# Performance work log

Hardware: AMD Instinct MI355X
Metric: run time of the kernel (lower is better)

## Reference

```python
import jax, jax.numpy as jnp
import numpy as np

# ExLoss constants (use_prior=False path)
T = 10.0
W_BU, W_H, W_TH = 1.0, 1.0, 3.0
P_MARGIN, N_MARGIN = 0.2, 0.3

B, C, D = 32, 40000, 2048


def setup_inputs() -> dict:
    key = jax.random.key(0)
    k1, k2, k3, k4 = jax.random.split(key, 4)
    inputs = jax.random.normal(k1, (B, D), dtype=jnp.float32)
    targets = jax.random.randint(k2, (B,), 0, 16)            # few identities -> positive pairs exist
    indexs = jax.random.randint(k3, (B,), 0, C)              # unused (use_prior=False)
    label_to_pairs = jnp.zeros((B,), dtype=jnp.int32)        # unused placeholder
    V = jax.random.normal(k4, (C, D), dtype=jnp.float32)
    V = V / jnp.linalg.norm(V, axis=1, keepdims=True)        # bank rows are L2-normalized by the EMA update
    return {"inputs": inputs, "V": V, "targets": targets,
            "label_to_pairs": label_to_pairs, "indexs": indexs}


def _masked_bce(logits, mask, target):
    # BCEWithLogits, reduction='mean' over masked elements; 0 if mask empty
    # per-elem: target*softplus(-x) + (1-target)*softplus(x)
    per = target * jax.nn.softplus(-logits) + (1.0 - target) * jax.nn.softplus(logits)
    cnt = jnp.sum(mask)
    s = jnp.sum(jnp.where(mask, per, 0.0))
    return jnp.where(cnt > 0, s / jnp.maximum(cnt, 1), 0.0)


def _ex_loss(inputs, V, targets):
    n = inputs.shape[0]
    # Exclusive: memory-bank matmul, scaled by t
    outputs = (inputs @ V.T) * T                                   # [B, C]
    # bu_loss: cross entropy (mean)
    logp = jax.nn.log_softmax(outputs, axis=1)
    bu_loss = -jnp.mean(jnp.take_along_axis(logp, targets[:, None], axis=1))

    # hard_negative_mining (batch sims, off-diagonal)
    ni = inputs / jnp.linalg.norm(inputs, axis=1, keepdims=True)
    sims = ni @ ni.T                                               # [B, B]
    eye = jnp.eye(n, dtype=bool)
    same = targets[:, None] == targets[None, :]
    pos = same & ~eye                                              # positive pairs, diag removed
    neg = ~same                                                    # negatives (diag is always 'same')
    # n_thrds: row min of psims BEFORE 2->-2 replacement (fill=2 where not positive)
    n_thrds = jnp.min(jnp.where(pos, sims, 2.0), axis=1, keepdims=True) - N_MARGIN
    # p_thrds: row max after 2->-2 replacement (fill=-2 where not positive)
    p_thrds = jnp.max(jnp.where(pos, sims, -2.0), axis=1, keepdims=True) - P_MARGIN
    hp_mask = pos & (sims < p_thrds)        # fill value 2 can never be < p_thrds (<= 0.8)
    hn_mask = neg & (sims > n_thrds)        # fill value -2 can never be > n_thrds
    h_loss = _masked_bce(sims, hp_mask, 1.0) + _masked_bce(sims, hn_mask, 0.0)

    # hard_negative_mining_with_table (only if no zero rows in V)
    active = jnp.all(jnp.sum(V, axis=1) != 0)
    nV = ni @ V.T                                                  # [B, C]
    n_th_t = jnp.take_along_axis(nV, targets[:, None], axis=1) - N_MARGIN  # [B,1]
    nsims_t = V[targets] @ V.T                                     # [B, C]
    t_mask = (n_th_t < nsims_t) & (nsims_t < 0.9999)
    th_loss = jnp.where(active, _masked_bce(nsims_t, t_mask, 0.0), 0.0)

    loss = W_BU * bu_loss + W_H * h_loss + W_TH * th_loss
    return loss, outputs


def reference(inputs, V, targets, label_to_pairs, indexs):
    # label_to_pairs / indexs unused: use_prior=False in ExLoss.__init__
    return _ex_loss(inputs, V, targets)
```

## Files before the change

### kernel.cpp

```cpp
#include <hip/hip_runtime.h>
#include <math.h>

#define B_ 32
#define C_ 40000
#define D_ 2048
#define T_SCALE 10.0f
#define P_MARG 0.2f
#define N_MARG 0.3f
#define NSTEP 64
#define KSPL 4
#define NCB 625
#define NBLK (NCB * KSPL)

typedef __attribute__((ext_vector_type(4))) float f32x4;
typedef __fp16 fp16x2 __attribute__((ext_vector_type(2)));
typedef _Float16 f16x2n __attribute__((ext_vector_type(2)));
typedef _Float16 half8_t __attribute__((ext_vector_type(8)));

#define OP1_OFF 0
#define OP_FLOATS (B_ * C_)
#define NS0_OFF (OP1_OFF + 3 * OP_FLOATS)
#define VR_OFF (NS0_OFF + 4 * OP_FLOATS)
#define VR_FLOATS C_
#define SC_OFF (VR_OFF + VR_FLOATS)
#define S_HLOSS 0
#define S_THSUM 1
#define S_THCNT 2
#define S_BAD 3
#define S_NTH 4
#define S_BU 36
#define SC_FLOATS 128
#define DT_OFF (SC_OFF + SC_FLOATS)
#define DT_FLOATS (32 * 32)
#define AF_OFF (DT_OFF + DT_FLOATS)
#define AF_FLOATS (NSTEP * 2048 / 2)
#define WS_FLOATS_TOTAL (AF_OFF + AF_FLOATS)

__device__ __forceinline__ float softplus_f(float x) {
    return (x > 0.f) ? (x + log1pf(expf(-x))) : log1pf(expf(x));
}

__device__ __forceinline__ void split_f16x2(float x0, float x1, unsigned& uh, unsigned& ul) {
    fp16x2 h = __builtin_amdgcn_cvt_pkrtz(x0, x1);
    float r0 = x0 - (float)h[0];
    float r1 = x1 - (float)h[1];
    fp16x2 lo = __builtin_amdgcn_cvt_pkrtz(r0, r1);
    uh = __builtin_bit_cast(unsigned, h);
    ul = __builtin_bit_cast(unsigned, lo);
}

__device__ __forceinline__ unsigned pack_rtne(float x0, float x1) {
    f16x2n p = {(_Float16)x0, (_Float16)x1};
    return __builtin_bit_cast(unsigned, p);
}

__global__ __launch_bounds__(256) void build_Afrag(const float* __restrict__ in,
                                                   const float* __restrict__ V,
                                                   const int* __restrict__ tgt,
                                                   unsigned short* __restrict__ Af) {
    int s = blockIdx.x;
    int f = threadIdx.x >> 6;
    int l = threadIdx.x & 63;
    int row = f * 16 + (l & 15);
    int k = s * 32 + (l >> 4) * 8;
    const float* src = (row < 32) ? (in + (size_t)row * D_ + k)
                                  : (V + (size_t)tgt[row - 32] * D_ + k);
    f32x4 x0 = *(const f32x4*)src;
    f32x4 x1 = *(const f32x4*)(src + 4);
    uint4 u = make_uint4(pack_rtne(x0[0], x0[1]), pack_rtne(x0[2], x0[3]),
                         pack_rtne(x1[0], x1[1]), pack_rtne(x1[2], x1[3]));
    *(uint4*)(Af + (size_t)s * 2048 + (size_t)f * 512 + (size_t)l * 8) = u;
}

__global__ __launch_bounds__(256) void sims_dots(const float* __restrict__ in,
                                                 float* __restrict__ dt) {
    __shared__ float part[8][32];
    int i = blockIdx.x;
    int j = threadIdx.x & 31;
    int sl = threadIdx.x >> 5;
    const float4* a4 = (const float4*)(in + (size_t)i * D_ + sl * 256);
    const float4* b4 = (const float4*)(in + (size_t)j * D_ + sl * 256);
    float s = 0.f;
#pragma unroll 4
    for (int k = 0; k < 64; ++k) {
        float4 x = a4[k], y = b4[k];
        s += x.x * y.x + x.y * y.y + x.z * y.z + x.w * y.w;
    }
    part[sl][j] = s;
    __syncthreads();
    if (threadIdx.x < 32) {
        float t = 0.f;
#pragma unroll
        for (int p = 0; p < 8; ++p) t += part[p][threadIdx.x];
        dt[i * 32 + threadIdx.x] = t;
    }
}

__global__ __launch_bounds__(1024) void small_finish(const float* __restrict__ in,
                                                     const float* __restrict__ V,
                                                     const int* __restrict__ tgt,
                                                     float* __restrict__ ws) {
    __shared__ float sims[32][33];
    __shared__ float nthr[32], pthr[32];
    __shared__ int ts[32];
    __shared__ float diag[32];
    __shared__ float red[4];
    int tid = threadIdx.x;
    int i = tid >> 5, j = tid & 31;
    const float* dt = ws + DT_OFF;
    if (tid < 32) { ts[tid] = tgt[tid]; diag[tid] = dt[tid * 32 + tid]; }
    if (tid < 4) red[tid] = 0.f;
    __syncthreads();
    float sim = dt[i * 32 + j] * rsqrtf(diag[i] * diag[j]);
    sims[i][j] = sim;
    __syncthreads();
    if (tid < 32) {
        float nmin = 2.f, pmax = -2.f;
        int ti = ts[tid];
        for (int jj = 0; jj < 32; ++jj) {
            bool pos = (ts[jj] == ti) && (jj != tid);
            float v = sims[tid][jj];
            if (pos) { nmin = fminf(nmin, v); pmax = fmaxf(pmax, v); }
        }
        nthr[tid] = nmin - N_MARG;
        pthr[tid] = pmax - P_MARG;
    }
    __syncthreads();
    bool pos = (ts[i] == ts[j]) && (i != j);
    bool neg = (ts[i] != ts[j]);
    if (pos && sim < pthr[i]) { atomicAdd(&red[0], softplus_f(-sim)); atomicAdd(&red[1], 1.f); }
    if (neg && sim > nthr[i]) { atomicAdd(&red[2], softplus_f(sim)); atomicAdd(&red[3], 1.f); }

    const float4* a4 = (const float4*)(in + (size_t)i * D_);
    const float4* v4 = (const float4*)(V + (size_t)ts[i] * D_);
    float sn = 0.f;
    for (int k = j; k < D_ / 4; k += 32) {
        float4 x = a4[k], y = v4[k];
        sn += x.x * y.x + x.y * y.y + x.z * y.z + x.w * y.w;
    }
    for (int off = 16; off > 0; off >>= 1) sn += __shfl_down(sn, off, 32);
    if (j == 0) ws[SC_OFF + S_NTH + i] = sn * rsqrtf(diag[i]) - N_MARG;
    __syncthreads();
    if (tid == 0) {
        float h = 0.f;
        if (red[1] > 0.f) h += red[0] / red[1];
        if (red[3] > 0.f) h += red[2] / red[3];
        ws[SC_OFF + S_HLOSS] = h;
    }
}

__global__ __launch_bounds__(256, 6) void gemm_mfma(const float* __restrict__ V,
                                                    const unsigned short* __restrict__ Af,
                                                    float* __restrict__ op0,
                                                    float* __restrict__ ws) {
    const int l = threadIdx.x & 63;
    const int w = threadIdx.x >> 6;
    const int ks = blockIdx.x / NCB;
    const int cb = blockIdx.x % NCB;
    const int col = l & 15, g = l >> 4;
    const int c = (cb * 4 + w) * 16 + col;

    const float* vp = V + (size_t)c * D_ + ks * 512 + g * 8;
    const unsigned short* ap = Af + (size_t)(ks * 16) * 2048 + (size_t)l * 8;

    f32x4 z = {0.f, 0.f, 0.f, 0.f};
    f32x4 acc0 = z, acc1 = z, acc2 = z, acc3 = z;
    float vsum = 0.f;

#pragma unroll
    for (int s = 0; s < 16; ++s) {
        const unsigned short* as = ap + (size_t)s * 2048;
        uint4 a0 = *(const uint4*)(as + 0 * 512);
        uint4 a1 = *(const uint4*)(as + 1 * 512);
        uint4 a2 = *(const uint4*)(as + 2 * 512);
        uint4 a3 = *(const uint4*)(as + 3 * 512);
        f32x4 v0 = *(const f32x4*)(vp + s * 32);
        f32x4 v1 = *(const f32x4*)(vp + s * 32 + 4);

        vsum += v0[0] + v0[1] + v0[2] + v0[3] + v1[0] + v1[1] + v1[2] + v1[3];
        unsigned uh0, ul0, uh1, ul1, uh2, ul2, uh3, ul3;
        split_f16x2(v0[0], v0[1], uh0, ul0);
        split_f16x2(v0[2], v0[3], uh1, ul1);
        split_f16x2(v1[0], v1[1], uh2, ul2);
        split_f16x2(v1[2], v1[3], uh3, ul3);
        half8_t bh = __builtin_bit_cast(half8_t, make_uint4(uh0, uh1, uh2, uh3));
        half8_t bl = __builtin_bit_cast(half8_t, make_uint4(ul0, ul1, ul2, ul3));
        half8_t A0h = __builtin_bit_cast(half8_t, a0);
        half8_t A1h = __builtin_bit_cast(half8_t, a1);
        half8_t A2h = __builtin_bit_cast(half8_t, a2);
        half8_t A3h = __builtin_bit_cast(half8_t, a3);

        acc0 = __builtin_amdgcn_mfma_f32_16x16x32_f16(A0h, bh, acc0, 0, 0, 0);
        acc1 = __builtin_amdgcn_mfma_f32_16x16x32_f16(A1h, bh, acc1, 0, 0, 0);
        acc2 = __builtin_amdgcn_mfma_f32_16x16x32_f16(A2h, bh, acc2, 0, 0, 0);
        acc3 = __builtin_amdgcn_mfma_f32_16x16x32_f16(A3h, bh, acc3, 0, 0, 0);
        acc0 = __builtin_amdgcn_mfma_f32_16x16x32_f16(A0h, bl, acc0, 0, 0, 0);
        acc1 = __builtin_amdgcn_mfma_f32_16x16x32_f16(A1h, bl, acc1, 0, 0, 0);
        acc2 = __builtin_amdgcn_mfma_f32_16x16x32_f16(A2h, bl, acc2, 0, 0, 0);
        acc3 = __builtin_amdgcn_mfma_f32_16x16x32_f16(A3h, bl, acc3, 0, 0, 0);
    }

    vsum += __shfl_xor(vsum, 16);
    vsum += __shfl_xor(vsum, 32);
    if (g == 0) atomicAdd(&ws[VR_OFF + c], vsum);

    float* op = (ks == 0) ? op0 : (ws + OP1_OFF + (size_t)(ks - 1) * OP_FLOATS);
    float* nsp = ws + NS0_OFF + (size_t)ks * OP_FLOATS;
#pragma unroll
    for (int r = 0; r < 4; ++r) {
        int rr = g * 4 + r;
        op[(size_t)rr * C_ + c] = acc0[r];
        op[(size_t)(16 + rr) * C_ + c] = acc1[r];
        nsp[(size_t)rr * C_ + c] = acc2[r];
        nsp[(size_t)(16 + rr) * C_ + c] = acc3[r];
    }
}

__global__ __launch_bounds__(1024) void lse_th_combine(float* __restrict__ out,
                                                       const int* __restrict__ tgt,
                                                       float* __restrict__ ws) {
    int b = blockIdx.x;
    int tid = threadIdx.x;
    __shared__ float sm[1024], ss[1024], sts[1024], stc[1024];
    __shared__ float xt;
    const float* p1 = ws + OP1_OFF + 0 * OP_FLOATS + (size_t)b * C_;
    const float* p2 = ws + OP1_OFF + 1 * OP_FLOATS + (size_t)b * C_;
    const float* p3 = ws + OP1_OFF + 2 * OP_FLOATS + (size_t)b * C_;
    const float* q0 = ws + NS0_OFF + 0 * OP_FLOATS + (size_t)b * C_;
    const float* q1 = ws + NS0_OFF + 1 * OP_FLOATS + (size_t)b * C_;
    const float* q2 = ws + NS0_OFF + 2 * OP_FLOATS + (size_t)b * C_;
    const float* q3 = ws + NS0_OFF + 3 * OP_FLOATS + (size_t)b * C_;
    float* orow = out + (size_t)b * C_;
    float nth = ws[SC_OFF + S_NTH + b];
    int tg = tgt[b];
    float m = -INFINITY, s = 0.f, ts = 0.f, tc = 0.f;
    for (int c = tid; c < C_; c += 1024) {
        float x = (orow[c] + p1[c] + p2[c] + p3[c]) * T_SCALE;
        orow[c] = x;
        if (c == tg) xt = x;
        float mn = fmaxf(m, x);
        s = s * expf(m - mn) + expf(x - mn);
        m = mn;
        float q = q0[c] + q1[c] + q2[c] + q3[c];
        if (q > nth && q < 0.9999f) { ts += softplus_f(q); tc += 1.f; }
    }
    sm[tid] = m; ss[tid] = s; sts[tid] = ts; stc[tid] = tc;
    __syncthreads();
    for (int st2 = 512; st2 > 0; st2 >>= 1) {
        if (tid < st2) {
            float m2 = sm[tid + st2], s2 = ss[tid + st2];
            float M = fmaxf(sm[tid], m2);
            ss[tid] = ss[tid] * expf(sm[tid] - M) + s2 * expf(m2 - M);
            sm[tid] = M;
            sts[tid] += sts[tid + st2];
            stc[tid] += stc[tid + st2];
        }
        __syncthreads();
    }
    if (tid == 0) {
        ws[SC_OFF + S_BU + b] = (sm[0] + logf(ss[0])) - xt;
        if (stc[0] != 0.f) {
            atomicAdd(&ws[SC_OFF + S_THSUM], sts[0]);
            atomicAdd(&ws[SC_OFF + S_THCNT], stc[0]);
        }
    }
}

__global__ __launch_bounds__(256) void vrow_check(const float* __restrict__ ws_c,
                                                  float* __restrict__ ws) {
    int c = blockIdx.x * 256 + threadIdx.x;
    if (c < C_ && ws_c[VR_OFF + c] == 0.0f) ws[SC_OFF + S_BAD] = 1.0f;
}

__global__ void finalize(const float* __restrict__ ws, float* __restrict__ out0) {
    if (threadIdx.x == 0 && blockIdx.x == 0) {
        float bu = 0.f;
        for (int b = 0; b < 32; ++b) bu += ws[SC_OFF + S_BU + b];
        bu /= 32.f;
        float h = ws[SC_OFF + S_HLOSS];
        float th = 0.f;
        float cnt = ws[SC_OFF + S_THCNT];
        if (ws[SC_OFF + S_BAD] == 0.f && cnt > 0.f) th = ws[SC_OFF + S_THSUM] / cnt;
        out0[0] = 1.0f * bu + 1.0f * h + 3.0f * th;
    }
}

extern "C" void kernel_launch(void* const* d_in, const int* in_sizes, int n_in,
                              void* d_out, int out_size, void* d_ws, size_t ws_size,
                              hipStream_t stream) {
    const float* in = (const float*)d_in[0];
    const float* V = (const float*)d_in[1];
    const int* tgt = (const int*)d_in[2];
    float* outp = (float*)d_out;
    float* ws = (float*)d_ws;
    unsigned short* Af = (unsigned short*)(ws + AF_OFF);

    (void)hipMemsetAsync((void*)(ws + VR_OFF), 0,
                         (size_t)(VR_FLOATS + SC_FLOATS) * sizeof(float), stream);

    build_Afrag<<<NSTEP, 256, 0, stream>>>(in, V, tgt, Af);
    sims_dots<<<32, 256, 0, stream>>>(in, ws + DT_OFF);
    small_finish<<<1, 1024, 0, stream>>>(in, V, tgt, ws);

    gemm_mfma<<<NBLK, 256, 0, stream>>>(V, Af, outp + 1, ws);

    lse_th_combine<<<B_, 1024, 0, stream>>>(outp + 1, tgt, ws);
    vrow_check<<<(C_ + 255) / 256, 256, 0, stream>>>(ws, ws);
    finalize<<<1, 64, 0, stream>>>(ws, outp);
}
```

Before: 227.2 us.

## Stage A fragments in LDS via global_load_lds and batch V loads

In the MFMA GEMM, the shared A operand (the 16 k-steps times 4 row blocks of fp16 activations) is now copied once per block into LDS with direct global-to-LDS loads, instead of every wave re-reading it from global memory. V loads are grouped into two batches of eight k-steps so more loads are in flight before the MFMAs use them. Launch bounds drop from 6 to 4 waves per SIMD, which gives more registers for the batched V values but lowers occupancy. The 64KB LDS per block also limits residency.

```diff
diff --git a/kernel.cpp b/kernel.cpp
--- a/kernel.cpp
+++ b/kernel.cpp
@@ -16,6 +16,11 @@
 typedef __fp16 fp16x2 __attribute__((ext_vector_type(2)));
 typedef _Float16 f16x2n __attribute__((ext_vector_type(2)));
 typedef _Float16 half8_t __attribute__((ext_vector_type(8)));
+
+#define GLL(gsrc, ldst)                                                          \
+    __builtin_amdgcn_global_load_lds(                                            \
+        (const __attribute__((address_space(1))) unsigned int*)(gsrc),           \
+        (__attribute__((address_space(3))) unsigned int*)(ldst), 16, 0, 0)
 
 #define OP1_OFF 0
 #define OP_FLOATS (B_ * C_)
@@ -149,10 +154,11 @@
     }
 }
 
-__global__ __launch_bounds__(256, 6) void gemm_mfma(const float* __restrict__ V,
+__global__ __launch_bounds__(256, 4) void gemm_mfma(const float* __restrict__ V,
                                                     const unsigned short* __restrict__ Af,
                                                     float* __restrict__ op0,
                                                     float* __restrict__ ws) {
+    __shared__ unsigned short Als[16][4][512];
     const int l = threadIdx.x & 63;
     const int w = threadIdx.x >> 6;
     const int ks = blockIdx.x / NCB;
@@ -161,43 +167,59 @@
     const int c = (cb * 4 + w) * 16 + col;
 
     const float* vp = V + (size_t)c * D_ + ks * 512 + g * 8;
-    const unsigned short* ap = Af + (size_t)(ks * 16) * 2048 + (size_t)l * 8;
+
+    {
+        const unsigned short* asrc =
+            Af + (size_t)(ks * 16) * 2048 + (size_t)w * 512 + (size_t)l * 8;
+#pragma unroll
+        for (int s = 0; s < 16; ++s) GLL(asrc + (size_t)s * 2048, &Als[s][w][0]);
+    }
+    __syncthreads();
 
     f32x4 z = {0.f, 0.f, 0.f, 0.f};
     f32x4 acc0 = z, acc1 = z, acc2 = z, acc3 = z;
     float vsum = 0.f;
 
 #pragma unroll
-    for (int s = 0; s < 16; ++s) {
-        const unsigned short* as = ap + (size_t)s * 2048;
-        uint4 a0 = *(const uint4*)(as + 0 * 512);
-        uint4 a1 = *(const uint4*)(as + 1 * 512);
-        uint4 a2 = *(const uint4*)(as + 2 * 512);
-        uint4 a3 = *(const uint4*)(as + 3 * 512);
-        f32x4 v0 = *(const f32x4*)(vp + s * 32);
-        f32x4 v1 = *(const f32x4*)(vp + s * 32 + 4);
-
-        vsum += v0[0] + v0[1] + v0[2] + v0[3] + v1[0] + v1[1] + v1[2] + v1[3];
-        unsigned uh0, ul0, uh1, ul1, uh2, ul2, uh3, ul3;
-        split_f16x2(v0[0], v0[1], uh0, ul0);
-        split_f16x2(v0[2], v0[3], uh1, ul1);
-        split_f16x2(v1[0], v1[1], uh2, ul2);
-        split_f16x2(v1[2], v1[3], uh3, ul3);
-        half8_t bh = __builtin_bit_cast(half8_t, make_uint4(uh0, uh1, uh2, uh3));
-        half8_t bl = __builtin_bit_cast(half8_t, make_uint4(ul0, ul1, ul2, ul3));
-        half8_t A0h = __builtin_bit_cast(half8_t, a0);
-        half8_t A1h = __builtin_bit_cast(half8_t, a1);
-        half8_t A2h = __builtin_bit_cast(half8_t, a2);
-        half8_t A3h = __builtin_bit_cast(half8_t, a3);
-
-        acc0 = __builtin_amdgcn_mfma_f32_16x16x32_f16(A0h, bh, acc0, 0, 0, 0);
-        acc1 = __builtin_amdgcn_mfma_f32_16x16x32_f16(A1h, bh, acc1, 0, 0, 0);
-        acc2 = __builtin_amdgcn_mfma_f32_16x16x32_f16(A2h, bh, acc2, 0, 0, 0);
-        acc3 = __builtin_amdgcn_mfma_f32_16x16x32_f16(A3h, bh, acc3, 0, 0, 0);
-        acc0 = __builtin_amdgcn_mfma_f32_16x16x32_f16(A0h, bl, acc0, 0, 0, 0);
-        acc1 = __builtin_amdgcn_mfma_f32_16x16x32_f16(A1h, bl, acc1, 0, 0, 0);
-        acc2 = __builtin_amdgcn_mfma_f32_16x16x32_f16(A2h, bl, acc2, 0, 0, 0);
-        acc3 = __builtin_amdgcn_mfma_f32_16x16x32_f16(A3h, bl, acc3, 0, 0, 0);
+    for (int h = 0; h < 2; ++h) {
+        f32x4 va[8], vb[8];
+#pragma unroll
+        for (int s = 0; s < 8; ++s) {
+            const float* p = vp + (h * 8 + s) * 32;
+            va[s] = *(const f32x4*)p;
+            vb[s] = *(const f32x4*)(p + 4);
+        }
+#pragma unroll
+        for (int s = 0; s < 8; ++s) {
+            const int st = h * 8 + s;
+            uint4 a0 = *(const uint4*)&Als[st][0][l * 8];
+            uint4 a1 = *(const uint4*)&Als[st][1][l * 8];
+            uint4 a2 = *(const uint4*)&Als[st][2][l * 8];
+            uint4 a3 = *(const uint4*)&Als[st][3][l * 8];
+            f32x4 v0 = va[s], v1 = vb[s];
+
+            vsum += v0[0] + v0[1] + v0[2] + v0[3] + v1[0] + v1[1] + v1[2] + v1[3];
+            unsigned uh0, ul0, uh1, ul1, uh2, ul2, uh3, ul3;
+            split_f16x2(v0[0], v0[1], uh0, ul0);
+            split_f16x2(v0[2], v0[3], uh1, ul1);
+            split_f16x2(v1[0], v1[1], uh2, ul2);
+            split_f16x2(v1[2], v1[3], uh3, ul3);
+            half8_t bh = __builtin_bit_cast(half8_t, make_uint4(uh0, uh1, uh2, uh3));
+            half8_t bl = __builtin_bit_cast(half8_t, make_uint4(ul0, ul1, ul2, ul3));
+            half8_t A0h = __builtin_bit_cast(half8_t, a0);
+            half8_t A1h = __builtin_bit_cast(half8_t, a1);
+            half8_t A2h = __builtin_bit_cast(half8_t, a2);
+            half8_t A3h = __builtin_bit_cast(half8_t, a3);
+
+            acc0 = __builtin_amdgcn_mfma_f32_16x16x32_f16(A0h, bh, acc0, 0, 0, 0);
+            acc1 = __builtin_amdgcn_mfma_f32_16x16x32_f16(A1h, bh, acc1, 0, 0, 0);
+            acc2 = __builtin_amdgcn_mfma_f32_16x16x32_f16(A2h, bh, acc2, 0, 0, 0);
+            acc3 = __builtin_amdgcn_mfma_f32_16x16x32_f16(A3h, bh, acc3, 0, 0, 0);
+            acc0 = __builtin_amdgcn_mfma_f32_16x16x32_f16(A0h, bl, acc0, 0, 0, 0);
+            acc1 = __builtin_amdgcn_mfma_f32_16x16x32_f16(A1h, bl, acc1, 0, 0, 0);
+            acc2 = __builtin_amdgcn_mfma_f32_16x16x32_f16(A2h, bl, acc2, 0, 0, 0);
+            acc3 = __builtin_amdgcn_mfma_f32_16x16x32_f16(A3h, bl, acc3, 0, 0, 0);
+        }
     }
 
     vsum += __shfl_xor(vsum, 16);
```

After: 212.1 us. -6.7%, faster.

## Drop split-fp16 low part for V and double-buffer GEMM loads

Applied to the files above, without the earlier changes.

The GEMM kernel stops splitting V into high and low fp16 halves and issues only the high-part MFMAs, halving matrix work and conversion ALU. The K loop is restructured into two register buffers of four steps each, so global loads run ahead of compute. Occupancy hint drops from 6 to 2 blocks per SIMD to fit the larger register footprint, and the block-index mapping now interleaves k-splits for adjacent column blocks. Dropping the low part reduces accuracy of the logits and the V@V products (rtz fp16 on V), which risks tolerance failures, especially on the nsims_t<0.9999 threshold.

```diff
diff --git a/kernel.cpp b/kernel.cpp
--- a/kernel.cpp
+++ b/kernel.cpp
@@ -40,13 +40,9 @@
     return (x > 0.f) ? (x + log1pf(expf(-x))) : log1pf(expf(x));
 }
 
-__device__ __forceinline__ void split_f16x2(float x0, float x1, unsigned& uh, unsigned& ul) {
+__device__ __forceinline__ unsigned pack_rtz(float x0, float x1) {
     fp16x2 h = __builtin_amdgcn_cvt_pkrtz(x0, x1);
-    float r0 = x0 - (float)h[0];
-    float r1 = x1 - (float)h[1];
-    fp16x2 lo = __builtin_amdgcn_cvt_pkrtz(r0, r1);
-    uh = __builtin_bit_cast(unsigned, h);
-    ul = __builtin_bit_cast(unsigned, lo);
+    return __builtin_bit_cast(unsigned, h);
 }
 
 __device__ __forceinline__ unsigned pack_rtne(float x0, float x1) {
@@ -149,16 +145,16 @@
     }
 }
 
-__global__ __launch_bounds__(256, 6) void gemm_mfma(const float* __restrict__ V,
+__global__ __launch_bounds__(256, 2) void gemm_mfma(const float* __restrict__ V,
                                                     const unsigned short* __restrict__ Af,
                                                     float* __restrict__ op0,
                                                     float* __restrict__ ws) {
     const int l = threadIdx.x & 63;
     const int w = threadIdx.x >> 6;
-    const int ks = blockIdx.x / NCB;
-    const int cb = blockIdx.x % NCB;
+    const int ks = blockIdx.x & 3;
+    const int cb = blockIdx.x >> 2;
     const int col = l & 15, g = l >> 4;
-    const int c = (cb * 4 + w) * 16 + col;
+    const int c = cb * 64 + w * 16 + col;
 
     const float* vp = V + (size_t)c * D_ + ks * 512 + g * 8;
     const unsigned short* ap = Af + (size_t)(ks * 16) * 2048 + (size_t)l * 8;
@@ -167,38 +163,48 @@
     f32x4 acc0 = z, acc1 = z, acc2 = z, acc3 = z;
     float vsum = 0.f;
 
-#pragma unroll
-    for (int s = 0; s < 16; ++s) {
-        const unsigned short* as = ap + (size_t)s * 2048;
-        uint4 a0 = *(const uint4*)(as + 0 * 512);
-        uint4 a1 = *(const uint4*)(as + 1 * 512);
-        uint4 a2 = *(const uint4*)(as + 2 * 512);
-        uint4 a3 = *(const uint4*)(as + 3 * 512);
-        f32x4 v0 = *(const f32x4*)(vp + s * 32);
-        f32x4 v1 = *(const f32x4*)(vp + s * 32 + 4);
-
-        vsum += v0[0] + v0[1] + v0[2] + v0[3] + v1[0] + v1[1] + v1[2] + v1[3];
-        unsigned uh0, ul0, uh1, ul1, uh2, ul2, uh3, ul3;
-        split_f16x2(v0[0], v0[1], uh0, ul0);
-        split_f16x2(v0[2], v0[3], uh1, ul1);
-        split_f16x2(v1[0], v1[1], uh2, ul2);
-        split_f16x2(v1[2], v1[3], uh3, ul3);
-        half8_t bh = __builtin_bit_cast(half8_t, make_uint4(uh0, uh1, uh2, uh3));
-        half8_t bl = __builtin_bit_cast(half8_t, make_uint4(ul0, ul1, ul2, ul3));
-        half8_t A0h = __builtin_bit_cast(half8_t, a0);
-        half8_t A1h = __builtin_bit_cast(half8_t, a1);
-        half8_t A2h = __builtin_bit_cast(half8_t, a2);
-        half8_t A3h = __builtin_bit_cast(half8_t, a3);
-
-        acc0 = __builtin_amdgcn_mfma_f32_16x16x32_f16(A0h, bh, acc0, 0, 0, 0);
-        acc1 = __builtin_amdgcn_mfma_f32_16x16x32_f16(A1h, bh, acc1, 0, 0, 0);
-        acc2 = __builtin_amdgcn_mfma_f32_16x16x32_f16(A2h, bh, acc2, 0, 0, 0);
-        acc3 = __builtin_amdgcn_mfma_f32_16x16x32_f16(A3h, bh, acc3, 0, 0, 0);
-        acc0 = __builtin_amdgcn_mfma_f32_16x16x32_f16(A0h, bl, acc0, 0, 0, 0);
-        acc1 = __builtin_amdgcn_mfma_f32_16x16x32_f16(A1h, bl, acc1, 0, 0, 0);
-        acc2 = __builtin_amdgcn_mfma_f32_16x16x32_f16(A2h, bl, acc2, 0, 0, 0);
-        acc3 = __builtin_amdgcn_mfma_f32_16x16x32_f16(A3h, bl, acc3, 0, 0, 0);
-    }
+    uint4 Aa[4][4], Ab[4][4];
+    f32x4 VaA[4], VbA[4], VaB[4], VbB[4];
+
+#define LOADB(AB, VA, VB, t0)                                      \
+    _Pragma("unroll") for (int s = 0; s < 4; ++s) {                \
+        const unsigned short* as = ap + (size_t)((t0) + s) * 2048; \
+        AB[s][0] = *(const uint4*)(as + 0 * 512);                  \
+        AB[s][1] = *(const uint4*)(as + 1 * 512);                  \
+        AB[s][2] = *(const uint4*)(as + 2 * 512);                  \
+        AB[s][3] = *(const uint4*)(as + 3 * 512);                  \
+        VA[s] = *(const f32x4*)(vp + ((t0) + s) * 32);             \
+        VB[s] = *(const f32x4*)(vp + ((t0) + s) * 32 + 4);         \
+    }
+
+#define COMPB(AB, VA, VB)                                                          \
+    _Pragma("unroll") for (int s = 0; s < 4; ++s) {                                \
+        f32x4 v0 = VA[s], v1 = VB[s];                                              \
+        vsum += v0[0] + v0[1] + v0[2] + v0[3] + v1[0] + v1[1] + v1[2] + v1[3];     \
+        uint4 bu = make_uint4(pack_rtz(v0[0], v0[1]), pack_rtz(v0[2], v0[3]),      \
+                              pack_rtz(v1[0], v1[1]), pack_rtz(v1[2], v1[3]));     \
+        half8_t bh = __builtin_bit_cast(half8_t, bu);                              \
+        half8_t A0h = __builtin_bit_cast(half8_t, AB[s][0]);                       \
+        half8_t A1h = __builtin_bit_cast(half8_t, AB[s][1]);                       \
+        half8_t A2h = __builtin_bit_cast(half8_t, AB[s][2]);                       \
+        half8_t A3h = __builtin_bit_cast(half8_t, AB[s][3]);                       \
+        acc0 = __builtin_amdgcn_mfma_f32_16x16x32_f16(A0h, bh, acc0, 0, 0, 0);     \
+        acc1 = __builtin_amdgcn_mfma_f32_16x16x32_f16(A1h, bh, acc1, 0, 0, 0);     \
+        acc2 = __builtin_amdgcn_mfma_f32_16x16x32_f16(A2h, bh, acc2, 0, 0, 0);     \
+        acc3 = __builtin_amdgcn_mfma_f32_16x16x32_f16(A3h, bh, acc3, 0, 0, 0);     \
+    }
+
+    LOADB(Aa, VaA, VbA, 0);
+    LOADB(Ab, VaB, VbB, 4);
+    COMPB(Aa, VaA, VbA);
+    LOADB(Aa, VaA, VbA, 8);
+    COMPB(Ab, VaB, VbB);
+    LOADB(Ab, VaB, VbB, 12);
+    COMPB(Aa, VaA, VbA);
+    COMPB(Ab, VaB, VbB);
+
+#undef LOADB
+#undef COMPB
 
     vsum += __shfl_xor(vsum, 16);
     vsum += __shfl_xor(vsum, 32);
```

Result: faster. 220.9 us (-2.8%).
